# Performance work log

Measured on AMD Instinct MI355X. Metric: run time of the kernel, lower is better.

Reference implementation:

```python
import jax, jax.numpy as jnp
import numpy as np

N, E_DIM, H, N_EDGES, OUT = 4096, 256, 4, 131072, 256


def _ln(x, g, b, eps=1e-5):
    m = x.mean(-1, keepdims=True)
    v = ((x - m) ** 2).mean(-1, keepdims=True)
    return (x - m) / jnp.sqrt(v + eps) * g + b


def _mha(q_in, kv_in, in_w, in_b, out_w, out_b, n_heads):
    # torch nn.MultiheadAttention with packed in_proj_weight [3E, E]
    e = q_in.shape[-1]
    dh = e // n_heads
    wq, wk, wv = jnp.split(in_w, 3, axis=0)
    bq, bk, bv = jnp.split(in_b, 3)
    q = (q_in @ wq.T + bq).reshape(-1, n_heads, dh)   # [N,H,Dh]
    k = (kv_in @ wk.T + bk).reshape(-1, n_heads, dh)
    v = (kv_in @ wv.T + bv).reshape(-1, n_heads, dh)
    scale = 1.0 / jnp.sqrt(jnp.asarray(dh, q.dtype))
    scores = jnp.einsum('nhd,mhd->hnm', q, k) * scale  # [H,N,M]
    attn = jax.nn.softmax(scores, axis=-1)
    o = jnp.einsum('hnm,mhd->nhd', attn, v).reshape(-1, e)
    return o @ out_w.T + out_b


def _gcn_conv(x, edge_index):
    # out[c] += (1/sqrt(d[c])) * (1/sqrt(d[r])) * x[r] for each edge (r,c),
    # d = in-degree counted on col; non-finite norms zeroed (nan_to_num)
    n = x.shape[0]
    row, col = edge_index[0], edge_index[1]
    d = jax.ops.segment_sum(jnp.ones_like(col, dtype=x.dtype), col, num_segments=n)
    dn = 1.0 / jnp.sqrt(d)
    value = dn[col] * dn[row]
    value = jnp.where(jnp.isfinite(value), value, 0.0)
    return jax.ops.segment_sum(value[:, None] * x[row], col, num_segments=n)


def setup_inputs() -> dict:
    key = jax.random.key(0)
    ks = jax.random.split(key, 12)
    s = 1.0 / np.sqrt(E_DIM)
    rn = lambda k, shape: jax.random.normal(k, shape, jnp.float32) * s
    return {
        'x': jax.random.normal(ks[0], (N, E_DIM), jnp.float32),
        'edge_index': jax.random.randint(ks[1], (2, N_EDGES), 0, N, dtype=jnp.int32),
        'weight_local': jax.random.uniform(ks[2], (E_DIM, E_DIM), jnp.float32, -s, s),
        'sa_in_w': rn(ks[3], (3 * E_DIM, E_DIM)),
        'sa_in_b': jnp.zeros((3 * E_DIM,), jnp.float32),
        'sa_out_w': rn(ks[4], (E_DIM, E_DIM)),
        'sa_out_b': jnp.zeros((E_DIM,), jnp.float32),
        'ln1_g': jnp.ones((E_DIM,), jnp.float32),
        'ln1_b': jnp.zeros((E_DIM,), jnp.float32),
        'ca_in_w': rn(ks[5], (3 * E_DIM, E_DIM)),
        'ca_in_b': jnp.zeros((3 * E_DIM,), jnp.float32),
        'ca_out_w': rn(ks[6], (E_DIM, E_DIM)),
        'ca_out_b': jnp.zeros((E_DIM,), jnp.float32),
        'ln2_g': jnp.ones((E_DIM,), jnp.float32),
        'ln2_b': jnp.zeros((E_DIM,), jnp.float32),
        'gate_w': rn(ks[7], (E_DIM, 2 * E_DIM)),
        'gate_b': jnp.zeros((E_DIM,), jnp.float32),
        'fc_w': rn(ks[8], (OUT, E_DIM)),
        'fc_b': jnp.zeros((OUT,), jnp.float32),
    }


def reference(x, edge_index, weight_local, sa_in_w, sa_in_b, sa_out_w, sa_out_b,
              ln1_g, ln1_b, ca_in_w, ca_in_b, ca_out_w, ca_out_b, ln2_g, ln2_b,
              gate_w, gate_b, fc_w, fc_b):
    hi = _gcn_conv(x, edge_index)                       # [N,E]
    local_embed = hi @ weight_local                     # [N,E]
    attn_out = _mha(x, x, sa_in_w, sa_in_b, sa_out_w, sa_out_b, H)
    global_embed = _ln(x + attn_out, ln1_g, ln1_b)      # [N,E]
    cross_out = _mha(global_embed, local_embed, ca_in_w, ca_in_b, ca_out_w, ca_out_b, H)
    aligned = _ln(global_embed + cross_out, ln2_g, ln2_b)
    concat = jnp.concatenate([global_embed, aligned], axis=-1)  # [N,2E]
    final_embed = jax.nn.relu(concat @ gate_w.T + gate_b)
    return final_embed @ fc_w.T + fc_b
```

## Files before the change

kernel.cpp:

```cpp
#include <hip/hip_runtime.h>
#include <hip/hip_bf16.h>

#define NN 4096
#define EDIM 256
#define NHEAD 4
#define DH 64
#define NEDGE 131072
#define NE (NN * EDIM)
#define NSPLIT 8
#define KEYS_PER_SPLIT (NN / NSPLIT)
#define QKS 512

typedef __bf16 bf16x8 __attribute__((ext_vector_type(8)));
typedef float f32x4 __attribute__((ext_vector_type(4)));
typedef float f32x16 __attribute__((ext_vector_type(16)));

__device__ inline void gload_lds16(const void* g, void* l) {
    __builtin_amdgcn_global_load_lds((const __attribute__((address_space(1))) unsigned int*)g,
                                     (__attribute__((address_space(3))) unsigned int*)l, 16, 0, 0);
}

__global__ __launch_bounds__(256) void prep_kernel(
    const float* __restrict__ wl, const float* __restrict__ siw, const float* __restrict__ sib,
    const float* __restrict__ sow, const float* __restrict__ ciw, const float* __restrict__ cib,
    const float* __restrict__ cow, const float* __restrict__ gw, const float* __restrict__ fw,
    const float* __restrict__ x,
    __bf16* __restrict__ siwb, __bf16* __restrict__ ciwb, __bf16* __restrict__ sowb,
    __bf16* __restrict__ cowb, __bf16* __restrict__ gwb, __bf16* __restrict__ fwb,
    __bf16* __restrict__ wlT, __bf16* __restrict__ xb,
    float* __restrict__ sib_adj, float* __restrict__ cib_adj) {
    long i = (long)blockIdx.x * 256 + threadIdx.x;
    if (i < 196608) { float v = siw[i]; if (i < 65536) v *= 0.125f; siwb[i] = (__bf16)v; return; }
    i -= 196608;
    if (i < 196608) { float v = ciw[i]; if (i < 65536) v *= 0.125f; ciwb[i] = (__bf16)v; return; }
    i -= 196608;
    if (i < 65536) { sowb[i] = (__bf16)sow[i]; return; }
    i -= 65536;
    if (i < 65536) { cowb[i] = (__bf16)cow[i]; return; }
    i -= 65536;
    if (i < 131072) { gwb[i] = (__bf16)gw[i]; return; }
    i -= 131072;
    if (i < 65536) { fwb[i] = (__bf16)fw[i]; return; }
    i -= 65536;
    if (i < 65536) { int n = (int)(i >> 8), k = (int)(i & 255); wlT[i] = (__bf16)wl[k * 256 + n]; return; }
    i -= 65536;
    if (i < 1048576) { xb[i] = (__bf16)x[i]; return; }
    i -= 1048576;
    if (i < 768) { sib_adj[i] = sib[i] * (i < 256 ? 0.125f : 1.f); return; }
    i -= 768;
    if (i < 768) { cib_adj[i] = cib[i] * (i < 256 ? 0.125f : 1.f); return; }
}

__global__ __launch_bounds__(256) void degi_kernel(const int* __restrict__ ei,
                                                   int* __restrict__ degi, int ne) {
    int e = blockIdx.x * 256 + threadIdx.x;
    if (e < ne) atomicAdd(&degi[ei[ne + e]], 1);
}

__global__ __launch_bounds__(256) void scan_kernel(const int* __restrict__ degi,
                                                   int* __restrict__ off,
                                                   int* __restrict__ cursor,
                                                   float* __restrict__ dnz) {
    __shared__ int s[256];
    const int t = threadIdx.x, i0 = t * 16;
    int v[16], sum = 0;
#pragma unroll
    for (int j = 0; j < 16; ++j) { v[j] = degi[i0 + j]; sum += v[j]; }
    s[t] = sum;
    __syncthreads();
#pragma unroll
    for (int d = 1; d < 256; d <<= 1) {
        int add = (t >= d) ? s[t - d] : 0;
        __syncthreads();
        s[t] += add;
        __syncthreads();
    }
    int base = s[t] - sum;
#pragma unroll
    for (int j = 0; j < 16; ++j) {
        off[i0 + j] = base;
        cursor[i0 + j] = base;
        dnz[i0 + j] = (v[j] > 0) ? rsqrtf((float)v[j]) : 0.f;
        base += v[j];
    }
}

__global__ __launch_bounds__(256) void fill_kernel(const int* __restrict__ ei,
                                                   int* __restrict__ cursor,
                                                   int* __restrict__ rows, int ne) {
    int e = blockIdx.x * 256 + threadIdx.x;
    if (e < ne) {
        int r = ei[e], c = ei[ne + e];
        int pos = atomicAdd(&cursor[c], 1);
        rows[pos] = r;
    }
}

__global__ __launch_bounds__(256) void gather_kernel(const int* __restrict__ off,
                                                     const int* __restrict__ rows,
                                                     const float* __restrict__ dnz,
                                                     const __bf16* __restrict__ xb,
                                                     __bf16* __restrict__ hib) {
    __shared__ float sm[2][256];
    const int c = blockIdx.x, t = threadIdx.x;
    const int half = t >> 7, c2 = (t & 127) * 2;
    const int s0 = off[c];
    const int s1 = (c == NN - 1) ? NEDGE : off[c + 1];
    float a0 = 0.f, a1 = 0.f;
    for (int j = s0 + half; j < s1; j += 2) {
        int r = rows[j];
        float dv = dnz[r];
        unsigned int pk = *(const unsigned int*)&xb[(size_t)r * EDIM + c2];
        a0 += dv * __uint_as_float(pk << 16);
        a1 += dv * __uint_as_float(pk & 0xffff0000u);
    }
    sm[half][c2] = a0;
    sm[half][c2 + 1] = a1;
    __syncthreads();
    float v = (sm[0][t] + sm[1][t]) * dnz[c];
    hib[(size_t)c * EDIM + t] = (__bf16)v;
}

__device__ inline void gemm_core(const __bf16* __restrict__ A, int lda,
                                 const __bf16* __restrict__ Bt, int ldb,
                                 int row0, int col0, int K, int tid,
                                 __bf16* As, __bf16* Bs, f32x4 acc[4]) {
    const int w = tid >> 6, l = tid & 63, lr = l & 15, lk = l >> 4;
    for (int k0 = 0; k0 < K; k0 += 64) {
        if (k0) __syncthreads();
#pragma unroll
        for (int cc = 0; cc < 2; ++cc) {
            int E0 = (w * 2 + cc) * 512;
            int row = (E0 >> 6) + (l >> 3);
            int col = (l & 7) * 8;
            int sc = col ^ ((row & 7) << 3);
            gload_lds16(A + (size_t)(row0 + row) * lda + k0 + sc, &As[E0]);
            gload_lds16(Bt + (size_t)(col0 + row) * ldb + k0 + sc, &Bs[E0]);
        }
        __syncthreads();
#pragma unroll
        for (int ks = 0; ks < 2; ++ks) {
            int cswz = (ks * 32 + lk * 8) ^ ((lr & 7) << 3);
            bf16x8 af = *(bf16x8*)&As[(w * 16 + lr) * 64 + cswz];
#pragma unroll
            for (int nt = 0; nt < 4; ++nt) {
                bf16x8 bfr = *(bf16x8*)&Bs[(nt * 16 + lr) * 64 + cswz];
                acc[nt] = __builtin_amdgcn_mfma_f32_16x16x32_bf16(af, bfr, acc[nt], 0, 0, 0);
            }
        }
    }
}

template <bool RELU, bool OUTBF>
__global__ __launch_bounds__(256) void gemm_bf16(const __bf16* __restrict__ A,
                                                 const __bf16* __restrict__ A2, int lda,
                                                 const __bf16* __restrict__ Bt, int ldb,
                                                 const float* __restrict__ bias,
                                                 void* __restrict__ Cv, int ldc, int K) {
    __shared__ __align__(16) __bf16 As[4096];
    __shared__ __align__(16) __bf16 Bs[4096];
    const int tid = threadIdx.x;
    const int row0 = blockIdx.y * 64, col0 = blockIdx.x * 64;
    const int w = tid >> 6, l = tid & 63, lr = l & 15, lk = l >> 4;
    f32x4 acc[4] = {};
    for (int k0 = 0; k0 < K; k0 += 64) {
        if (k0) __syncthreads();
        const __bf16* Asrc = A;
        int ka = k0;
        if (A2 != nullptr && k0 >= 256) { Asrc = A2; ka = k0 - 256; }
#pragma unroll
        for (int cc = 0; cc < 2; ++cc) {
            int E0 = (w * 2 + cc) * 512;
            int row = (E0 >> 6) + (l >> 3);
            int col = (l & 7) * 8;
            int sc = col ^ ((row & 7) << 3);
            gload_lds16(Asrc + (size_t)(row0 + row) * lda + ka + sc, &As[E0]);
            gload_lds16(Bt + (size_t)(col0 + row) * ldb + k0 + sc, &Bs[E0]);
        }
        __syncthreads();
#pragma unroll
        for (int ks = 0; ks < 2; ++ks) {
            int cswz = (ks * 32 + lk * 8) ^ ((lr & 7) << 3);
            bf16x8 af = *(bf16x8*)&As[(w * 16 + lr) * 64 + cswz];
#pragma unroll
            for (int nt = 0; nt < 4; ++nt) {
                bf16x8 bfr = *(bf16x8*)&Bs[(nt * 16 + lr) * 64 + cswz];
                acc[nt] = __builtin_amdgcn_mfma_f32_16x16x32_bf16(af, bfr, acc[nt], 0, 0, 0);
            }
        }
    }
#pragma unroll
    for (int nt = 0; nt < 4; ++nt) {
        float bv = bias ? bias[col0 + nt * 16 + lr] : 0.f;
#pragma unroll
        for (int r = 0; r < 4; ++r) {
            float v = acc[nt][r] + bv;
            if (RELU) v = fmaxf(v, 0.f);
            size_t ci = (size_t)(row0 + w * 16 + lk * 4 + r) * ldc + col0 + nt * 16 + lr;
            if (OUTBF) ((__bf16*)Cv)[ci] = (__bf16)v;
            else ((float*)Cv)[ci] = v;
        }
    }
}

__device__ inline void qkv_epilogue(f32x4 acc[4], const float* __restrict__ bias,
                                    int gcol0, int row0, int tid,
                                    __bf16* __restrict__ qkv, __bf16* __restrict__ vtb) {
    const int w = tid >> 6, l = tid & 63, lr = l & 15, lk = l >> 4;
    if (gcol0 < 512) {
#pragma unroll
        for (int nt = 0; nt < 4; ++nt) {
            float bv = bias[gcol0 + nt * 16 + lr];
#pragma unroll
            for (int r = 0; r < 4; ++r)
                qkv[(size_t)(row0 + w * 16 + lk * 4 + r) * QKS + gcol0 + nt * 16 + lr] =
                    (__bf16)(acc[nt][r] + bv);
        }
    } else {
        const int n4 = row0 + w * 16 + lk * 4;
#pragma unroll
        for (int nt = 0; nt < 4; ++nt) {
            int dg = gcol0 - 512 + nt * 16 + lr;
            float bv = bias[gcol0 + nt * 16 + lr];
            union { __bf16 b[4]; ushort4 u; } pk;
#pragma unroll
            for (int r = 0; r < 4; ++r) pk.b[r] = (__bf16)(acc[nt][r] + bv);
            *(ushort4*)&vtb[(size_t)dg * NN + n4] = pk.u;
        }
    }
}

__global__ __launch_bounds__(256) void fused_local_qkv(
    const __bf16* __restrict__ hi_bf, const __bf16* __restrict__ x_bf,
    const __bf16* __restrict__ wlT, const __bf16* __restrict__ siwb,
    const float* __restrict__ sib,
    __bf16* __restrict__ local_bf, __bf16* __restrict__ qkv, __bf16* __restrict__ vtb) {
    __shared__ __align__(16) __bf16 As[4096];
    __shared__ __align__(16) __bf16 Bs[4096];
    const int tid = threadIdx.x;
    const int bx = blockIdx.x, row0 = blockIdx.y * 64;
    f32x4 acc[4] = {};
    if (bx < 4) {
        gemm_core(hi_bf, 256, wlT, 256, row0, bx * 64, 256, tid, As, Bs, acc);
        const int w = tid >> 6, l = tid & 63, lr = l & 15, lk = l >> 4;
#pragma unroll
        for (int nt = 0; nt < 4; ++nt)
#pragma unroll
            for (int r = 0; r < 4; ++r)
                local_bf[(size_t)(row0 + w * 16 + lk * 4 + r) * 256 + bx * 64 + nt * 16 + lr] =
                    (__bf16)acc[nt][r];
    } else {
        const int gcol0 = (bx - 4) * 64;
        gemm_core(x_bf, 256, siwb, 256, row0, gcol0, 256, tid, As, Bs, acc);
        qkv_epilogue(acc, sib, gcol0, row0, tid, qkv, vtb);
    }
}

__global__ __launch_bounds__(256) void fused_cross_proj(
    const __bf16* __restrict__ global_bf, const __bf16* __restrict__ local_bf,
    const __bf16* __restrict__ ciwb, const float* __restrict__ cib,
    __bf16* __restrict__ qkv, __bf16* __restrict__ vtb) {
    __shared__ __align__(16) __bf16 As[4096];
    __shared__ __align__(16) __bf16 Bs[4096];
    const int tid = threadIdx.x;
    const int bx = blockIdx.x, row0 = blockIdx.y * 64;
    const int gcol0 = (bx < 4) ? bx * 64 : 256 + (bx - 4) * 64;
    const __bf16* A = (bx < 4) ? global_bf : local_bf;
    f32x4 acc[4] = {};
    gemm_core(A, 256, ciwb, 256, row0, gcol0, 256, tid, As, Bs, acc);
    qkv_epilogue(acc, cib, gcol0, row0, tid, qkv, vtb);
}

__global__ __launch_bounds__(256, 4) void attn_split(const __bf16* __restrict__ qkvb,
                                                     const __bf16* __restrict__ Vtb,
                                                     __bf16* __restrict__ p0,
                                                     __bf16* __restrict__ p1,
                                                     __bf16* __restrict__ p2,
                                                     __bf16* __restrict__ p3,
                                                     float* __restrict__ ml) {
    const int h = blockIdx.y, s = blockIdx.z;
    const int n0 = blockIdx.x * 128;
    const int tid = threadIdx.x;
    const int w = tid >> 6, l = tid & 63;
    const int qi = l & 31, hi = l >> 5, hi8 = hi * 8;
    const int swz = (l & 7) << 3;

    __shared__ __align__(16) __bf16 Kt[4096];
    __shared__ __align__(16) __bf16 Vt[4096];

    const int qrow = n0 + w * 32 + qi;
    bf16x8 qf[4];
#pragma unroll
    for (int d0 = 0; d0 < 4; ++d0)
        qf[d0] = *(const bf16x8*)&qkvb[(size_t)qrow * QKS + h * 64 + d0 * 16 + hi8];

    f32x16 ot0 = {}, ot1 = {};
    float sum_part = 0.f;
    const __bf16* Vbh = Vtb + (size_t)h * 64 * NN;

    for (int t = 0; t < KEYS_PER_SPLIT / 64; ++t) {
        const int kv0 = s * KEYS_PER_SPLIT + t * 64;
        __syncthreads();
#pragma unroll
        for (int cc = 0; cc < 2; ++cc) {
            int E0 = (w * 2 + cc) * 512;
            int row = (E0 >> 6) + (l >> 3);
            int col = (l & 7) * 8;
            int sc = col ^ ((row & 7) << 3);
            gload_lds16(qkvb + (size_t)(kv0 + row) * QKS + 256 + h * 64 + sc, &Kt[E0]);
            gload_lds16(Vbh + (size_t)row * NN + kv0 + sc, &Vt[E0]);
        }
        __syncthreads();

#pragma unroll
        for (int ss = 0; ss < 2; ++ss) {
            f32x16 st = {};
#pragma unroll
            for (int d0 = 0; d0 < 4; ++d0) {
                bf16x8 kf = *(bf16x8*)&Kt[(ss * 32 + qi) * 64 + ((d0 * 16 + hi8) ^ swz)];
                st = __builtin_amdgcn_mfma_f32_32x32x16_bf16(kf, qf[d0], st, 0, 0, 0);
            }
            float p_[16];
#pragma unroll
            for (int r = 0; r < 16; ++r) {
                p_[r] = __expf(fminf(st[r], 30.f));
                sum_part += p_[r];
            }
            unsigned int wd[8];
#pragma unroll
            for (int j = 0; j < 8; ++j)
                asm("v_cvt_pk_bf16_f32 %0, %1, %2" : "=v"(wd[j]) : "v"(p_[2 * j]), "v"(p_[2 * j + 1]));
            asm("v_permlane32_swap_b32 %0, %1" : "+v"(wd[0]), "+v"(wd[2]));
            asm("v_permlane32_swap_b32 %0, %1" : "+v"(wd[1]), "+v"(wd[3]));
            asm("v_permlane32_swap_b32 %0, %1" : "+v"(wd[4]), "+v"(wd[6]));
            asm("v_permlane32_swap_b32 %0, %1" : "+v"(wd[5]), "+v"(wd[7]));
            union { unsigned int u[4]; bf16x8 v; } pa0, pa1;
            pa0.u[0] = wd[0]; pa0.u[1] = wd[1]; pa0.u[2] = wd[2]; pa0.u[3] = wd[3];
            pa1.u[0] = wd[4]; pa1.u[1] = wd[5]; pa1.u[2] = wd[6]; pa1.u[3] = wd[7];
#pragma unroll
            for (int kt = 0; kt < 2; ++kt) {
                bf16x8 pav = kt ? pa1.v : pa0.v;
                int colk = (ss * 32 + kt * 16 + hi8) ^ swz;
                bf16x8 vf0 = *(bf16x8*)&Vt[qi * 64 + colk];
                bf16x8 vf1 = *(bf16x8*)&Vt[(32 + qi) * 64 + colk];
                ot0 = __builtin_amdgcn_mfma_f32_32x32x16_bf16(vf0, pav, ot0, 0, 0, 0);
                ot1 = __builtin_amdgcn_mfma_f32_32x32x16_bf16(vf1, pav, ot1, 0, 0, 0);
            }
        }
    }

    float tot = sum_part + __shfl_xor(sum_part, 32);
    __bf16* pb;
    switch (s >> 1) {
        case 0: pb = p0; break;
        case 1: pb = p1; break;
        case 2: pb = p2; break;
        default: pb = p3; break;
    }
    pb += (size_t)(s & 1) * NN * 256;
    __bf16* dst = &pb[(size_t)qrow * 256 + h * 64];
#pragma unroll
    for (int r = 0; r < 16; r += 2) {
        int d = (r & 3) + 8 * (r >> 2) + 4 * hi;
        union { unsigned int u; __bf16 b[2]; } w2;
        w2.b[0] = (__bf16)ot0[r]; w2.b[1] = (__bf16)ot0[r + 1];
        *(unsigned int*)&dst[d] = w2.u;
        union { unsigned int u; __bf16 b[2]; } w3;
        w3.b[0] = (__bf16)ot1[r]; w3.b[1] = (__bf16)ot1[r + 1];
        *(unsigned int*)&dst[32 + d] = w3.u;
    }
    if (hi == 0) ml[((size_t)s * NHEAD + h) * NN + qrow] = tot;
}

__global__ __launch_bounds__(256) void attn_merge(const __bf16* __restrict__ p0,
                                                  const __bf16* __restrict__ p1,
                                                  const __bf16* __restrict__ p2,
                                                  const __bf16* __restrict__ p3,
                                                  const float* __restrict__ ml,
                                                  __bf16* __restrict__ coreb) {
    int idx = blockIdx.x * 256 + threadIdx.x;
    int n = idx >> 8, c = idx & 255, h = c >> 6;
    float L = 0.f, O = 0.f;
#pragma unroll
    for (int s = 0; s < NSPLIT; ++s) {
        const __bf16* pb = (s < 2 ? p0 : s < 4 ? p1 : s < 6 ? p2 : p3) + (size_t)(s & 1) * NN * 256;
        O += (float)pb[(size_t)n * 256 + c];
        L += ml[((size_t)s * NHEAD + h) * NN + n];
    }
    coreb[idx] = (__bf16)(O / L);
}

__device__ inline float block_sum256(float v, float* tmp) {
#pragma unroll
    for (int o = 32; o; o >>= 1) v += __shfl_xor(v, o);
    __syncthreads();
    if ((threadIdx.x & 63) == 0) tmp[threadIdx.x >> 6] = v;
    __syncthreads();
    return tmp[0] + tmp[1] + tmp[2] + tmp[3];
}

__global__ __launch_bounds__(256) void ln_kernel(const float* __restrict__ a,
                                                 const float* __restrict__ b,
                                                 const float* __restrict__ g,
                                                 const float* __restrict__ be,
                                                 float* __restrict__ outf,
                                                 __bf16* __restrict__ outb) {
    __shared__ float tmp[4];
    const int n = blockIdx.x, t = threadIdx.x;
    float v = a[n * EDIM + t] + b[n * EDIM + t];
    float mean = block_sum256(v, tmp) * (1.f / 256.f);
    float c = v - mean;
    float var = block_sum256(c * c, tmp) * (1.f / 256.f);
    float o = c * (1.f / sqrtf(var + 1e-5f)) * g[t] + be[t];
    if (outf) outf[n * EDIM + t] = o;
    if (outb) outb[n * EDIM + t] = (__bf16)o;
}

extern "C" void kernel_launch(void* const* d_in, const int* in_sizes, int n_in,
                              void* d_out, int out_size, void* d_ws, size_t ws_size,
                              hipStream_t stream) {
    const float* x = (const float*)d_in[0];
    const int* ei = (const int*)d_in[1];
    const float* w_local = (const float*)d_in[2];
    const float* sa_in_w = (const float*)d_in[3];
    const float* sa_in_b = (const float*)d_in[4];
    const float* sa_out_w = (const float*)d_in[5];
    const float* sa_out_b = (const float*)d_in[6];
    const float* ln1_g = (const float*)d_in[7];
    const float* ln1_b = (const float*)d_in[8];
    const float* ca_in_w = (const float*)d_in[9];
    const float* ca_in_b = (const float*)d_in[10];
    const float* ca_out_w = (const float*)d_in[11];
    const float* ca_out_b = (const float*)d_in[12];
    const float* ln2_g = (const float*)d_in[13];
    const float* ln2_b = (const float*)d_in[14];
    const float* gate_w = (const float*)d_in[15];
    const float* gate_b = (const float*)d_in[16];
    const float* fc_w = (const float*)d_in[17];
    const float* fc_b = (const float*)d_in[18];
    float* out = (float*)d_out;

    float* ws = (float*)d_ws;
    float* dnz = ws;
    float* ml = ws + 4096;
    __bf16* x_bf = (__bf16*)(ml + 131072);
    __bf16* hi_bf = (__bf16*)((float*)x_bf + NE / 2);
    __bf16* local_bf = (__bf16*)((float*)hi_bf + NE / 2);
    __bf16* qkv_bf = (__bf16*)((float*)local_bf + NE / 2);
    __bf16* core_bf = (__bf16*)((float*)qkv_bf + 3 * NE / 2);
    float* proj = (float*)core_bf + NE / 2;
    float* global_f = proj + NE;
    __bf16* global_bf = (__bf16*)(global_f + NE);
    __bf16* aligned_bf = (__bf16*)((float*)global_bf + NE / 2);
    __bf16* fin_bf = (__bf16*)((float*)aligned_bf + NE / 2);
    __bf16* vtb = (__bf16*)((float*)fin_bf + NE / 2);
    __bf16* siwb = (__bf16*)((float*)vtb + NE / 2);
    __bf16* ciwb = siwb + 196608;
    __bf16* sowb = ciwb + 196608;
    __bf16* cowb = sowb + 65536;
    __bf16* gwb = cowb + 65536;
    __bf16* fwb = gwb + 131072;
    __bf16* wlT = fwb + 65536;
    float* sib_adj = (float*)(wlT + 65536);
    float* cib_adj = sib_adj + 768;

    int* degi = (int*)qkv_bf;
    int* off = degi + 4096;
    int* cursor = off + 4096;
    int* rows = cursor + 4096;

    __bf16* pA = (__bf16*)out;
    __bf16* pB = x_bf;
    __bf16* pC = (__bf16*)proj;
    __bf16* pD = aligned_bf;

    prep_kernel<<<7174, 256, 0, stream>>>(w_local, sa_in_w, sa_in_b, sa_out_w,
                                          ca_in_w, ca_in_b, ca_out_w, gate_w, fc_w, x,
                                          siwb, ciwb, sowb, cowb, gwb, fwb, wlT, x_bf,
                                          sib_adj, cib_adj);

    hipMemsetAsync(degi, 0, 4096 * sizeof(int), stream);
    degi_kernel<<<NEDGE / 256, 256, 0, stream>>>(ei, degi, NEDGE);
    scan_kernel<<<1, 256, 0, stream>>>(degi, off, cursor, dnz);
    fill_kernel<<<NEDGE / 256, 256, 0, stream>>>(ei, cursor, rows, NEDGE);
    gather_kernel<<<NN, 256, 0, stream>>>(off, rows, dnz, x_bf, hi_bf);

    fused_local_qkv<<<dim3(16, 64), 256, 0, stream>>>(
        hi_bf, x_bf, wlT, siwb, sib_adj, local_bf, qkv_bf, vtb);
    attn_split<<<dim3(NN / 128, NHEAD, NSPLIT), 256, 0, stream>>>(qkv_bf, vtb, pA, pB, pC, pD, ml);
    attn_merge<<<4096, 256, 0, stream>>>(pA, pB, pC, pD, ml, core_bf);
    gemm_bf16<false, false><<<dim3(4, 64), 256, 0, stream>>>(
        core_bf, nullptr, 256, sowb, 256, sa_out_b, proj, 256, 256);
    ln_kernel<<<NN, 256, 0, stream>>>(x, proj, ln1_g, ln1_b, global_f, global_bf);

    fused_cross_proj<<<dim3(12, 64), 256, 0, stream>>>(
        global_bf, local_bf, ciwb, cib_adj, qkv_bf, vtb);
    attn_split<<<dim3(NN / 128, NHEAD, NSPLIT), 256, 0, stream>>>(qkv_bf, vtb, pA, pB, pC, pD, ml);
    attn_merge<<<4096, 256, 0, stream>>>(pA, pB, pC, pD, ml, core_bf);
    gemm_bf16<false, false><<<dim3(4, 64), 256, 0, stream>>>(
        core_bf, nullptr, 256, cowb, 256, ca_out_b, proj, 256, 256);
    ln_kernel<<<NN, 256, 0, stream>>>(global_f, proj, ln2_g, ln2_b, nullptr, aligned_bf);

    gemm_bf16<true, true><<<dim3(4, 64), 256, 0, stream>>>(
        global_bf, aligned_bf, 256, gwb, 512, gate_b, fin_bf, 256, 512);
    gemm_bf16<false, false><<<dim3(4, 64), 256, 0, stream>>>(
        fin_bf, nullptr, 256, fwb, 256, fc_b, out, 256, 256);
}
```

Measured before the change: 174.9 us.

## Double-buffer LDS tiles in GEMM and attention loops, fold degree memset into prep

Adds ping-pong LDS buffers to the bf16 GEMM core, the standalone GEMM, the fused projection kernels and split attention, so the next K/KV tile's global-to-LDS load is issued before computing on the current one. This removes one barrier per iteration and hides load latency. It also zeroes the degree array inside the prep kernel instead of with a separate memset, and removes the clamp before exp in attention. The costs are doubled shared memory per block, which may lower occupancy, and a possible overflow risk from the unclamped exponent.

```diff
diff --git a/kernel.cpp b/kernel.cpp
--- a/kernel.cpp
+++ b/kernel.cpp
@@ -28,7 +28,7 @@
     __bf16* __restrict__ siwb, __bf16* __restrict__ ciwb, __bf16* __restrict__ sowb,
     __bf16* __restrict__ cowb, __bf16* __restrict__ gwb, __bf16* __restrict__ fwb,
     __bf16* __restrict__ wlT, __bf16* __restrict__ xb,
-    float* __restrict__ sib_adj, float* __restrict__ cib_adj) {
+    float* __restrict__ sib_adj, float* __restrict__ cib_adj, int* __restrict__ degi) {
     long i = (long)blockIdx.x * 256 + threadIdx.x;
     if (i < 196608) { float v = siw[i]; if (i < 65536) v *= 0.125f; siwb[i] = (__bf16)v; return; }
     i -= 196608;
@@ -49,6 +49,8 @@
     if (i < 768) { sib_adj[i] = sib[i] * (i < 256 ? 0.125f : 1.f); return; }
     i -= 768;
     if (i < 768) { cib_adj[i] = cib[i] * (i < 256 ? 0.125f : 1.f); return; }
+    i -= 768;
+    if (i < 4096) degi[i] = 0;
 }
 
 __global__ __launch_bounds__(256) void degi_kernel(const int* __restrict__ ei,
@@ -126,28 +128,34 @@
                                  int row0, int col0, int K, int tid,
                                  __bf16* As, __bf16* Bs, f32x4 acc[4]) {
     const int w = tid >> 6, l = tid & 63, lr = l & 15, lk = l >> 4;
-    for (int k0 = 0; k0 < K; k0 += 64) {
-        if (k0) __syncthreads();
+    const int srow = (l >> 3), scol = (l & 7) * 8;
+    auto stage = [&](int k0, int buf) {
 #pragma unroll
         for (int cc = 0; cc < 2; ++cc) {
             int E0 = (w * 2 + cc) * 512;
-            int row = (E0 >> 6) + (l >> 3);
-            int col = (l & 7) * 8;
-            int sc = col ^ ((row & 7) << 3);
-            gload_lds16(A + (size_t)(row0 + row) * lda + k0 + sc, &As[E0]);
-            gload_lds16(Bt + (size_t)(col0 + row) * ldb + k0 + sc, &Bs[E0]);
-        }
-        __syncthreads();
+            int row = (E0 >> 6) + srow;
+            int sc = scol ^ ((row & 7) << 3);
+            gload_lds16(A + (size_t)(row0 + row) * lda + k0 + sc, &As[buf * 4096 + E0]);
+            gload_lds16(Bt + (size_t)(col0 + row) * ldb + k0 + sc, &Bs[buf * 4096 + E0]);
+        }
+    };
+    stage(0, 0);
+    __syncthreads();
+    int buf = 0;
+    for (int k0 = 0; k0 < K; k0 += 64) {
+        if (k0 + 64 < K) stage(k0 + 64, buf ^ 1);
 #pragma unroll
         for (int ks = 0; ks < 2; ++ks) {
             int cswz = (ks * 32 + lk * 8) ^ ((lr & 7) << 3);
-            bf16x8 af = *(bf16x8*)&As[(w * 16 + lr) * 64 + cswz];
+            bf16x8 af = *(bf16x8*)&As[buf * 4096 + (w * 16 + lr) * 64 + cswz];
 #pragma unroll
             for (int nt = 0; nt < 4; ++nt) {
-                bf16x8 bfr = *(bf16x8*)&Bs[(nt * 16 + lr) * 64 + cswz];
+                bf16x8 bfr = *(bf16x8*)&Bs[buf * 4096 + (nt * 16 + lr) * 64 + cswz];
                 acc[nt] = __builtin_amdgcn_mfma_f32_16x16x32_bf16(af, bfr, acc[nt], 0, 0, 0);
             }
         }
+        __syncthreads();
+        buf ^= 1;
     }
 }
 
@@ -157,37 +165,43 @@
                                                  const __bf16* __restrict__ Bt, int ldb,
                                                  const float* __restrict__ bias,
                                                  void* __restrict__ Cv, int ldc, int K) {
-    __shared__ __align__(16) __bf16 As[4096];
-    __shared__ __align__(16) __bf16 Bs[4096];
+    __shared__ __align__(16) __bf16 As[2 * 4096];
+    __shared__ __align__(16) __bf16 Bs[2 * 4096];
     const int tid = threadIdx.x;
     const int row0 = blockIdx.y * 64, col0 = blockIdx.x * 64;
     const int w = tid >> 6, l = tid & 63, lr = l & 15, lk = l >> 4;
+    const int srow = (l >> 3), scol = (l & 7) * 8;
     f32x4 acc[4] = {};
-    for (int k0 = 0; k0 < K; k0 += 64) {
-        if (k0) __syncthreads();
+    auto stage = [&](int k0, int buf) {
         const __bf16* Asrc = A;
         int ka = k0;
         if (A2 != nullptr && k0 >= 256) { Asrc = A2; ka = k0 - 256; }
 #pragma unroll
         for (int cc = 0; cc < 2; ++cc) {
             int E0 = (w * 2 + cc) * 512;
-            int row = (E0 >> 6) + (l >> 3);
-            int col = (l & 7) * 8;
-            int sc = col ^ ((row & 7) << 3);
-            gload_lds16(Asrc + (size_t)(row0 + row) * lda + ka + sc, &As[E0]);
-            gload_lds16(Bt + (size_t)(col0 + row) * ldb + k0 + sc, &Bs[E0]);
-        }
-        __syncthreads();
+            int row = (E0 >> 6) + srow;
+            int sc = scol ^ ((row & 7) << 3);
+            gload_lds16(Asrc + (size_t)(row0 + row) * lda + ka + sc, &As[buf * 4096 + E0]);
+            gload_lds16(Bt + (size_t)(col0 + row) * ldb + k0 + sc, &Bs[buf * 4096 + E0]);
+        }
+    };
+    stage(0, 0);
+    __syncthreads();
+    int buf = 0;
+    for (int k0 = 0; k0 < K; k0 += 64) {
+        if (k0 + 64 < K) stage(k0 + 64, buf ^ 1);
 #pragma unroll
         for (int ks = 0; ks < 2; ++ks) {
             int cswz = (ks * 32 + lk * 8) ^ ((lr & 7) << 3);
-            bf16x8 af = *(bf16x8*)&As[(w * 16 + lr) * 64 + cswz];
+            bf16x8 af = *(bf16x8*)&As[buf * 4096 + (w * 16 + lr) * 64 + cswz];
 #pragma unroll
             for (int nt = 0; nt < 4; ++nt) {
-                bf16x8 bfr = *(bf16x8*)&Bs[(nt * 16 + lr) * 64 + cswz];
+                bf16x8 bfr = *(bf16x8*)&Bs[buf * 4096 + (nt * 16 + lr) * 64 + cswz];
                 acc[nt] = __builtin_amdgcn_mfma_f32_16x16x32_bf16(af, bfr, acc[nt], 0, 0, 0);
             }
         }
+        __syncthreads();
+        buf ^= 1;
     }
 #pragma unroll
     for (int nt = 0; nt < 4; ++nt) {
@@ -235,8 +249,8 @@
     const __bf16* __restrict__ wlT, const __bf16* __restrict__ siwb,
     const float* __restrict__ sib,
     __bf16* __restrict__ local_bf, __bf16* __restrict__ qkv, __bf16* __restrict__ vtb) {
-    __shared__ __align__(16) __bf16 As[4096];
-    __shared__ __align__(16) __bf16 Bs[4096];
+    __shared__ __align__(16) __bf16 As[2 * 4096];
+    __shared__ __align__(16) __bf16 Bs[2 * 4096];
     const int tid = threadIdx.x;
     const int bx = blockIdx.x, row0 = blockIdx.y * 64;
     f32x4 acc[4] = {};
@@ -260,8 +274,8 @@
     const __bf16* __restrict__ global_bf, const __bf16* __restrict__ local_bf,
     const __bf16* __restrict__ ciwb, const float* __restrict__ cib,
     __bf16* __restrict__ qkv, __bf16* __restrict__ vtb) {
-    __shared__ __align__(16) __bf16 As[4096];
-    __shared__ __align__(16) __bf16 Bs[4096];
+    __shared__ __align__(16) __bf16 As[2 * 4096];
+    __shared__ __align__(16) __bf16 Bs[2 * 4096];
     const int tid = threadIdx.x;
     const int bx = blockIdx.x, row0 = blockIdx.y * 64;
     const int gcol0 = (bx < 4) ? bx * 64 : 256 + (bx - 4) * 64;
@@ -285,8 +299,8 @@
     const int qi = l & 31, hi = l >> 5, hi8 = hi * 8;
     const int swz = (l & 7) << 3;
 
-    __shared__ __align__(16) __bf16 Kt[4096];
-    __shared__ __align__(16) __bf16 Vt[4096];
+    __shared__ __align__(16) __bf16 Kt[2 * 4096];
+    __shared__ __align__(16) __bf16 Vt[2 * 4096];
 
     const int qrow = n0 + w * 32 + qi;
     bf16x8 qf[4];
@@ -297,33 +311,37 @@
     f32x16 ot0 = {}, ot1 = {};
     float sum_part = 0.f;
     const __bf16* Vbh = Vtb + (size_t)h * 64 * NN;
-
-    for (int t = 0; t < KEYS_PER_SPLIT / 64; ++t) {
+    const int srow = (l >> 3), scol = (l & 7) * 8;
+
+    auto stageKV = [&](int t, int buf) {
         const int kv0 = s * KEYS_PER_SPLIT + t * 64;
-        __syncthreads();
 #pragma unroll
         for (int cc = 0; cc < 2; ++cc) {
             int E0 = (w * 2 + cc) * 512;
-            int row = (E0 >> 6) + (l >> 3);
-            int col = (l & 7) * 8;
-            int sc = col ^ ((row & 7) << 3);
-            gload_lds16(qkvb + (size_t)(kv0 + row) * QKS + 256 + h * 64 + sc, &Kt[E0]);
-            gload_lds16(Vbh + (size_t)row * NN + kv0 + sc, &Vt[E0]);
-        }
-        __syncthreads();
-
+            int row = (E0 >> 6) + srow;
+            int sc = scol ^ ((row & 7) << 3);
+            gload_lds16(qkvb + (size_t)(kv0 + row) * QKS + 256 + h * 64 + sc, &Kt[buf * 4096 + E0]);
+            gload_lds16(Vbh + (size_t)row * NN + kv0 + sc, &Vt[buf * 4096 + E0]);
+        }
+    };
+
+    stageKV(0, 0);
+    __syncthreads();
+    int buf = 0;
+    for (int t = 0; t < KEYS_PER_SPLIT / 64; ++t) {
+        if (t + 1 < KEYS_PER_SPLIT / 64) stageKV(t + 1, buf ^ 1);
 #pragma unroll
         for (int ss = 0; ss < 2; ++ss) {
             f32x16 st = {};
 #pragma unroll
             for (int d0 = 0; d0 < 4; ++d0) {
-                bf16x8 kf = *(bf16x8*)&Kt[(ss * 32 + qi) * 64 + ((d0 * 16 + hi8) ^ swz)];
+                bf16x8 kf = *(bf16x8*)&Kt[buf * 4096 + (ss * 32 + qi) * 64 + ((d0 * 16 + hi8) ^ swz)];
                 st = __builtin_amdgcn_mfma_f32_32x32x16_bf16(kf, qf[d0], st, 0, 0, 0);
             }
             float p_[16];
 #pragma unroll
             for (int r = 0; r < 16; ++r) {
-                p_[r] = __expf(fminf(st[r], 30.f));
+                p_[r] = __expf(st[r]);
                 sum_part += p_[r];
             }
             unsigned int wd[8];
@@ -341,12 +359,14 @@
             for (int kt = 0; kt < 2; ++kt) {
                 bf16x8 pav = kt ? pa1.v : pa0.v;
                 int colk = (ss * 32 + kt * 16 + hi8) ^ swz;
-                bf16x8 vf0 = *(bf16x8*)&Vt[qi * 64 + colk];
-                bf16x8 vf1 = *(bf16x8*)&Vt[(32 + qi) * 64 + colk];
+                bf16x8 vf0 = *(bf16x8*)&Vt[buf * 4096 + qi * 64 + colk];
+                bf16x8 vf1 = *(bf16x8*)&Vt[buf * 4096 + (32 + qi) * 64 + colk];
                 ot0 = __builtin_amdgcn_mfma_f32_32x32x16_bf16(vf0, pav, ot0, 0, 0, 0);
                 ot1 = __builtin_amdgcn_mfma_f32_32x32x16_bf16(vf1, pav, ot1, 0, 0, 0);
             }
         }
+        __syncthreads();
+        buf ^= 1;
     }
 
     float tot = sum_part + __shfl_xor(sum_part, 32);
@@ -474,12 +494,11 @@
     __bf16* pC = (__bf16*)proj;
     __bf16* pD = aligned_bf;
 
-    prep_kernel<<<7174, 256, 0, stream>>>(w_local, sa_in_w, sa_in_b, sa_out_w,
+    prep_kernel<<<7190, 256, 0, stream>>>(w_local, sa_in_w, sa_in_b, sa_out_w,
                                           ca_in_w, ca_in_b, ca_out_w, gate_w, fc_w, x,
                                           siwb, ciwb, sowb, cowb, gwb, fwb, wlT, x_bf,
-                                          sib_adj, cib_adj);
-
-    hipMemsetAsync(degi, 0, 4096 * sizeof(int), stream);
+                                          sib_adj, cib_adj, degi);
+
     degi_kernel<<<NEDGE / 256, 256, 0, stream>>>(ei, degi, NEDGE);
     scan_kernel<<<1, 256, 0, stream>>>(degi, off, cursor, dnz);
     fill_kernel<<<NEDGE / 256, 256, 0, stream>>>(ei, cursor, rows, NEDGE);
```

Result: no change. 173.9 us (-0.6%).
